# Performance work log

Measured on AMD Instinct MI355X. Metric: run time of the kernel, lower is better.

The kernel has to match this reference:

```python
import math
import jax, jax.numpy as jnp
import numpy as np

H = 1024
N2 = 32  # N // 2
L_LEN = 4096


def setup_inputs() -> dict:
    key = jax.random.key(0)
    k0, k1, k2 = jax.random.split(key, 3)
    log_dt = jax.random.uniform(k0, (H,), dtype=jnp.float32) * (
        math.log(0.1) - math.log(0.001)) + math.log(0.001)
    C_real = jax.random.normal(k1, (H, N2), dtype=jnp.float32)
    C_imag = jax.random.normal(k2, (H, N2), dtype=jnp.float32)
    log_A_real = jnp.log(0.5 * jnp.ones((H, N2), dtype=jnp.float32))
    A_imag = math.pi * jnp.tile(jnp.arange(N2, dtype=jnp.float32)[None, :], (H, 1))
    return {
        "log_dt": log_dt,
        "C_real": C_real,
        "C_imag": C_imag,
        "log_A_real": log_A_real,
        "A_imag": A_imag,
        "L": L_LEN,
    }


def reference(log_dt, C_real, C_imag, log_A_real, A_imag, L):
    dt = jnp.exp(log_dt)                                   # [H]
    A = -jnp.exp(log_A_real) + 1j * A_imag                 # [H, N2] complex
    dtA = A * dt[:, None]                                  # [H, N2]
    l = jnp.arange(L, dtype=jnp.float32)                   # [L]
    Kexp = jnp.exp(dtA[:, :, None] * l)                    # [H, N2, L] complex (Vandermonde)
    Ct = (C_real + 1j * C_imag) * (jnp.exp(dtA) - 1.0) / A  # [H, N2]
    K = 2.0 * jnp.einsum('hn,hnl->hl', Ct, Kexp).real      # [H, L]
    return K
```

## Files before the change

kernel.cpp:

```cpp
#include <hip/hip_runtime.h>


#define N2    32
#define NPAIR (N2 / 2)
#define LLEN  4096
#define BLK   256
#define CL    (LLEN / BLK)
#define PCH   4
#define TOL   1e-3f

typedef float v2f __attribute__((ext_vector_type(2)));

__global__ __launch_bounds__(BLK, 4) void s4d_kernel(
    const float* __restrict__ log_dt,
    const float* __restrict__ C_real,
    const float* __restrict__ C_imag,
    const float* __restrict__ log_A_real,
    const float* __restrict__ A_imag,
    float* __restrict__ out)
{
    const int h = blockIdx.x;
    const int t = threadIdx.x;

    __shared__ v2f    sT0[N2][16];
    __shared__ float4 sU1[N2][16];
    __shared__ v2f    s2A[NPAIR];
    __shared__ v2f    sMR2[NPAIR];
    __shared__ v2f    sCt[N2];
    __shared__ float  sDrl2[N2];
    __shared__ double sTrev[N2];
    __shared__ float  sS, sRmax, sDrmax;
    __shared__ int    sJcut;

    if (t < N2) {
        const int n = t;
        const float dt = __expf(log_dt[h]);
        const float aR = -__expf(log_A_real[h * N2 + n]);
        const float aI = A_imag[h * N2 + n];
        const float dR = aR * dt;

        const double trev = (double)aI * (double)dt * 0.15915494309189535;

        double pz = trev; pz -= floor(pz);
        const float e1 = __expf(dR);
        const float zr = e1 * __builtin_amdgcn_cosf((float)pz);
        const float zi = e1 * __builtin_amdgcn_sinf((float)pz);

        const float inv = 1.0f / (aR * aR + aI * aI);
        const float nr  = zr - 1.0f;
        const float qr  = (nr * aR + zi * aI) * inv;
        const float qi  = (zi * aR - nr * aI) * inv;
        const float c_r = C_real[h * N2 + n], c_i = C_imag[h * N2 + n];
        const float Ctr = c_r * qr - c_i * qi;
        const float Cti = c_r * qi + c_i * qr;

        double p256 = trev * 256.0; p256 -= floor(p256);
        const float ew = __expf(dR * 256.0f);
        const float wx = ew * __builtin_amdgcn_cosf((float)p256);
        const float r2 = ew * ew;
        const float drl2 = dR * 1.4426950408889634f;

        sCt[n]   = (v2f){Ctr, Cti};
        sDrl2[n] = drl2;
        sTrev[n] = trev;
        ((float*)s2A)[n]  = 2.0f * wx;
        ((float*)sMR2)[n] = -r2;

        float S = fabsf(Ctr) + fabsf(Cti);
        float r = ew;
        float dm = drl2;
#pragma unroll
        for (int m = 16; m >= 1; m >>= 1) {
            S  += __shfl_xor(S, m, 32);
            r   = fmaxf(r,  __shfl_xor(r,  m, 32));
            dm  = fmaxf(dm, __shfl_xor(dm, m, 32));
        }
        if (n == 0) {
            sS = S; sRmax = r; sDrmax = dm;
            int jc = CL;
            if (r < 0.9999f) {
                const float tail0 = 2.0f * S / (1.0f - r);
                jc = 0;
                float rj = 1.0f;
                while (jc < CL && tail0 * rj >= TOL) { rj *= r; ++jc; }
            }
            sJcut = jc;
        }
    }
    __syncthreads();

#pragma unroll
    for (int it = 0; it < 4; ++it) {
        const int tau = t + BLK * it;
        if (tau < 512) {
            const int n = tau >> 4, k = tau & 15;
            double p = sTrev[n] * (double)k; p -= floor(p);
            const float g = __builtin_amdgcn_exp2f(sDrl2[n] * (float)k);
            sT0[n][k] = (v2f){ g * __builtin_amdgcn_cosf((float)p),
                               g * __builtin_amdgcn_sinf((float)p) };
        } else {
            const int tu = tau - 512;
            const int n = tu >> 4, m = tu & 15;
            const v2f    Ct = sCt[n];
            const double tr = sTrev[n];
            const float  dl = sDrl2[n];

            double p0 = tr * (double)(16 * m); p0 -= floor(p0);
            const float g0 = __builtin_amdgcn_exp2f(dl * (float)(16 * m));
            const float c0 = g0 * __builtin_amdgcn_cosf((float)p0);
            const float s0 = g0 * __builtin_amdgcn_sinf((float)p0);

            double p1 = tr * (double)(16 * m + 256); p1 -= floor(p1);
            const float g1 = __builtin_amdgcn_exp2f(dl * (float)(16 * m + 256));
            const float c1 = g1 * __builtin_amdgcn_cosf((float)p1);
            const float s1 = g1 * __builtin_amdgcn_sinf((float)p1);

            sU1[n][m] = make_float4(Ct.x * c0 - Ct.y * s0,
                                    Ct.x * s0 + Ct.y * c0,
                                    Ct.x * c1 - Ct.y * s1,
                                    Ct.x * s1 + Ct.y * c1);
        }
    }
    __syncthreads();

    v2f acc[CL];
#pragma unroll
    for (int j = 0; j < CL; ++j) acc[j] = (v2f){0.0f, 0.0f};

    const int jcut = __builtin_amdgcn_readfirstlane(sJcut);
    bool active = (jcut > 0);
    {
        const float rmax = sRmax;
        if (rmax < 0.9999f) {
            const float bound = 2.0f * sS *
                __builtin_amdgcn_exp2f(sDrmax * (float)t) / (1.0f - rmax);
            if (bound < TOL) active = false;
        }
    }

    if (active) {
        const int t0 = t & 15, t1 = t >> 4;

        for (int p0 = 0; p0 < NPAIR; p0 += PCH) {
            v2f xa[PCH], xb[PCH], c2a[PCH], cmr[PCH];

#pragma unroll
            for (int k = 0; k < PCH; ++k) {
                const int pair = p0 + k;
                c2a[k] = s2A[pair];
                cmr[k] = sMR2[pair];
#pragma unroll
                for (int e = 0; e < 2; ++e) {
                    const int n = 2 * pair + e;
                    const v2f    b = sT0[n][t0];
                    const float4 u = sU1[n][t1];
                    const float x0 = __builtin_fmaf(-u.y, b.y, u.x * b.x);
                    const float x1 = __builtin_fmaf(-u.w, b.y, u.z * b.x);
                    if (e == 0) { xa[k].x = x0; xb[k].x = x1; }
                    else        { xa[k].y = x0; xb[k].y = x1; }
                }
            }

#pragma unroll
            for (int k = 0; k < PCH; ++k) acc[0] += xa[k];
            if (jcut > 1) {
#pragma unroll
                for (int k = 0; k < PCH; ++k) acc[1] += xb[k];
            }

#pragma unroll
            for (int jp = 0; jp < (CL - 2) / 2; ++jp) {
                const int j = 2 + 2 * jp;
                if (j < jcut) {
#pragma unroll
                    for (int k = 0; k < PCH; ++k) {
                        xa[k] = c2a[k] * xb[k] + cmr[k] * xa[k];
                        acc[j] += xa[k];
                    }
#pragma unroll
                    for (int k = 0; k < PCH; ++k) {
                        xb[k] = c2a[k] * xa[k] + cmr[k] * xb[k];
                        acc[j + 1] += xb[k];
                    }
                }
            }
        }
    }

    float* __restrict__ o = out + (size_t)h * LLEN + t;
#pragma unroll
    for (int j = 0; j < CL; ++j) o[j * BLK] = 2.0f * (acc[j].x + acc[j].y);
}

extern "C" void kernel_launch(void* const* d_in, const int* in_sizes, int n_in,
                              void* d_out, int out_size, void* d_ws, size_t ws_size,
                              hipStream_t stream) {
    const float* log_dt     = (const float*)d_in[0];
    const float* C_real     = (const float*)d_in[1];
    const float* C_imag     = (const float*)d_in[2];
    const float* log_A_real = (const float*)d_in[3];
    const float* A_imag     = (const float*)d_in[4];
    float* out = (float*)d_out;

    const int H = in_sizes[0];
    s4d_kernel<<<dim3(H), dim3(BLK), 0, stream>>>(
        log_dt, C_real, C_imag, log_A_real, A_imag, out);
}
```

Before: 78.14 us.

## Split modes across two thread halves per block and reduce via shared memory

Doubles the block to 512 threads. Each half handles 16 of the 32 modes for the same 256 output positions, using a scalar per-mode recurrence in place of the paired v2f packing. The partial sums are combined through a shared-memory buffer, and each half then writes half of the outputs. The aim is more parallelism per head and shorter serial recurrence chains per thread, at the cost of an extra reduction, two more barriers and more shared memory.

New measurement: 88.24 us. +12.9%, slower.

```diff
diff --git a/kernel.cpp b/kernel.cpp
--- a/kernel.cpp
+++ b/kernel.cpp
@@ -2,16 +2,15 @@
 
 
 #define N2    32
-#define NPAIR (N2 / 2)
 #define LLEN  4096
-#define BLK   256
-#define CL    (LLEN / BLK)
-#define PCH   4
+#define BLK   512
+#define TQ    256
+#define CL    16
 #define TOL   1e-3f
 
 typedef float v2f __attribute__((ext_vector_type(2)));
 
-__global__ __launch_bounds__(BLK, 4) void s4d_kernel(
+__global__ __launch_bounds__(BLK, 8) void s4d_kernel(
     const float* __restrict__ log_dt,
     const float* __restrict__ C_real,
     const float* __restrict__ C_imag,
@@ -19,21 +18,23 @@
     const float* __restrict__ A_imag,
     float* __restrict__ out)
 {
-    const int h = blockIdx.x;
-    const int t = threadIdx.x;
+    const int h   = blockIdx.x;
+    const int tid = threadIdx.x;
+    const int t   = tid & (TQ - 1);
+    const int sl  = tid >> 8;
 
     __shared__ v2f    sT0[N2][16];
     __shared__ float4 sU1[N2][16];
-    __shared__ v2f    s2A[NPAIR];
-    __shared__ v2f    sMR2[NPAIR];
+    __shared__ v2f    sAB[N2];
     __shared__ v2f    sCt[N2];
     __shared__ float  sDrl2[N2];
     __shared__ double sTrev[N2];
+    __shared__ float  sRed[CL][TQ];
     __shared__ float  sS, sRmax, sDrmax;
     __shared__ int    sJcut;
 
-    if (t < N2) {
-        const int n = t;
+    if (tid < N2) {
+        const int n = tid;
         const float dt = __expf(log_dt[h]);
         const float aR = -__expf(log_A_real[h * N2 + n]);
         const float aI = A_imag[h * N2 + n];
@@ -63,8 +64,7 @@
         sCt[n]   = (v2f){Ctr, Cti};
         sDrl2[n] = drl2;
         sTrev[n] = trev;
-        ((float*)s2A)[n]  = 2.0f * wx;
-        ((float*)sMR2)[n] = -r2;
+        sAB[n]   = (v2f){2.0f * wx, -r2};
 
         float S = fabsf(Ctr) + fabsf(Cti);
         float r = ew;
@@ -90,8 +90,8 @@
     __syncthreads();
 
 #pragma unroll
-    for (int it = 0; it < 4; ++it) {
-        const int tau = t + BLK * it;
+    for (int it = 0; it < 2; ++it) {
+        const int tau = tid + BLK * it;
         if (tau < 512) {
             const int n = tau >> 4, k = tau & 15;
             double p = sTrev[n] * (double)k; p -= floor(p);
@@ -123,9 +123,9 @@
     }
     __syncthreads();
 
-    v2f acc[CL];
-#pragma unroll
-    for (int j = 0; j < CL; ++j) acc[j] = (v2f){0.0f, 0.0f};
+    float acc[CL];
+#pragma unroll
+    for (int j = 0; j < CL; ++j) acc[j] = 0.0f;
 
     const int jcut = __builtin_amdgcn_readfirstlane(sJcut);
     bool active = (jcut > 0);
@@ -140,32 +140,28 @@
 
     if (active) {
         const int t0 = t & 15, t1 = t >> 4;
-
-        for (int p0 = 0; p0 < NPAIR; p0 += PCH) {
-            v2f xa[PCH], xb[PCH], c2a[PCH], cmr[PCH];
-
-#pragma unroll
-            for (int k = 0; k < PCH; ++k) {
-                const int pair = p0 + k;
-                c2a[k] = s2A[pair];
-                cmr[k] = sMR2[pair];
-#pragma unroll
-                for (int e = 0; e < 2; ++e) {
-                    const int n = 2 * pair + e;
-                    const v2f    b = sT0[n][t0];
-                    const float4 u = sU1[n][t1];
-                    const float x0 = __builtin_fmaf(-u.y, b.y, u.x * b.x);
-                    const float x1 = __builtin_fmaf(-u.w, b.y, u.z * b.x);
-                    if (e == 0) { xa[k].x = x0; xb[k].x = x1; }
-                    else        { xa[k].y = x0; xb[k].y = x1; }
-                }
-            }
-
-#pragma unroll
-            for (int k = 0; k < PCH; ++k) acc[0] += xa[k];
+        const int nbase = sl * 16;
+
+        for (int ch = 0; ch < 2; ++ch) {
+            const int nb = nbase + ch * 8;
+            float xa[8], xb[8], ca[8], cb[8];
+
+#pragma unroll
+            for (int k = 0; k < 8; ++k) {
+                const int n = nb + k;
+                const v2f    b = sT0[n][t0];
+                const float4 u = sU1[n][t1];
+                xa[k] = __builtin_fmaf(-u.y, b.y, u.x * b.x);
+                xb[k] = __builtin_fmaf(-u.w, b.y, u.z * b.x);
+                const v2f ab = sAB[n];
+                ca[k] = ab.x;  cb[k] = ab.y;
+            }
+
+#pragma unroll
+            for (int k = 0; k < 8; ++k) acc[0] += xa[k];
             if (jcut > 1) {
 #pragma unroll
-                for (int k = 0; k < PCH; ++k) acc[1] += xb[k];
+                for (int k = 0; k < 8; ++k) acc[1] += xb[k];
             }
 
 #pragma unroll
@@ -173,13 +169,13 @@
                 const int j = 2 + 2 * jp;
                 if (j < jcut) {
 #pragma unroll
-                    for (int k = 0; k < PCH; ++k) {
-                        xa[k] = c2a[k] * xb[k] + cmr[k] * xa[k];
+                    for (int k = 0; k < 8; ++k) {
+                        xa[k] = ca[k] * xb[k] + cb[k] * xa[k];
                         acc[j] += xa[k];
                     }
 #pragma unroll
-                    for (int k = 0; k < PCH; ++k) {
-                        xb[k] = c2a[k] * xa[k] + cmr[k] * xb[k];
+                    for (int k = 0; k < 8; ++k) {
+                        xb[k] = ca[k] * xa[k] + cb[k] * xb[k];
                         acc[j + 1] += xb[k];
                     }
                 }
@@ -187,9 +183,21 @@
         }
     }
 
-    float* __restrict__ o = out + (size_t)h * LLEN + t;
-#pragma unroll
-    for (int j = 0; j < CL; ++j) o[j * BLK] = 2.0f * (acc[j].x + acc[j].y);
+    if (sl == 0) {
+#pragma unroll
+        for (int j = 0; j < CL; ++j) sRed[j][t] = acc[j];
+    }
+    __syncthreads();
+    if (sl == 1) {
+#pragma unroll
+        for (int j = 0; j < CL; ++j) sRed[j][t] += acc[j];
+    }
+    __syncthreads();
+
+    float* __restrict__ o = out + (size_t)h * LLEN + sl * (8 * TQ) + t;
+#pragma unroll
+    for (int jj = 0; jj < 8; ++jj)
+        o[jj * TQ] = 2.0f * sRed[8 * sl + jj][t];
 }
 
 extern "C" void kernel_launch(void* const* d_in, const int* in_sizes, int n_in,
```

## Split each channel's sequence across two blocks and repack shared tables

Applied to the files above, without the earlier changes.

Launches two blocks per channel, each covering half of the output length, so there are twice as many blocks and each thread needs fewer accumulators, which allows higher occupancy (launch bounds raised to 6). Each block writes its half directly as zeros when the decay cutoff excludes it. U1 entries for the second step are now derived by multiplying by the 256-step rotation instead of a second transcendental evaluation. Shared tables are repacked into float4 pairs so loads are wider. The cost is that both halves repeat the per-channel setup and table construction.

Result: slower. 80.74 us (+3.3%).

```diff
diff --git a/kernel.cpp b/kernel.cpp
--- a/kernel.cpp
+++ b/kernel.cpp
@@ -1,17 +1,16 @@
 #include <hip/hip_runtime.h>
 
 
-#define N2    32
-#define NPAIR (N2 / 2)
 #define LLEN  4096
 #define BLK   256
-#define CL    (LLEN / BLK)
-#define PCH   4
+#define N2    32
+#define NPR   16
+#define JPB   8
 #define TOL   1e-3f
 
 typedef float v2f __attribute__((ext_vector_type(2)));
 
-__global__ __launch_bounds__(BLK, 4) void s4d_kernel(
+__global__ __launch_bounds__(BLK, 6) void s4d_kernel(
     const float* __restrict__ log_dt,
     const float* __restrict__ C_real,
     const float* __restrict__ C_imag,
@@ -19,14 +18,16 @@
     const float* __restrict__ A_imag,
     float* __restrict__ out)
 {
-    const int h = blockIdx.x;
-    const int t = threadIdx.x;
-
-    __shared__ v2f    sT0[N2][16];
+    const int bx   = blockIdx.x;
+    const int h    = bx >> 1;
+    const int half = bx & 1;
+    const int joff = half * JPB;
+    const int t    = threadIdx.x;
+
+    __shared__ float4 sT0P[NPR][16];
     __shared__ float4 sU1[N2][16];
-    __shared__ v2f    s2A[NPAIR];
-    __shared__ v2f    sMR2[NPAIR];
-    __shared__ v2f    sCt[N2];
+    __shared__ float4 sABP[NPR];
+    __shared__ v2f    sCt[N2], sW[N2];
     __shared__ float  sDrl2[N2];
     __shared__ double sTrev[N2];
     __shared__ float  sS, sRmax, sDrmax;
@@ -57,17 +58,20 @@
         double p256 = trev * 256.0; p256 -= floor(p256);
         const float ew = __expf(dR * 256.0f);
         const float wx = ew * __builtin_amdgcn_cosf((float)p256);
+        const float wy = ew * __builtin_amdgcn_sinf((float)p256);
         const float r2 = ew * ew;
         const float drl2 = dR * 1.4426950408889634f;
 
         sCt[n]   = (v2f){Ctr, Cti};
+        sW[n]    = (v2f){wx, wy};
         sDrl2[n] = drl2;
         sTrev[n] = trev;
-        ((float*)s2A)[n]  = 2.0f * wx;
-        ((float*)sMR2)[n] = -r2;
-
-        float S = fabsf(Ctr) + fabsf(Cti);
-        float r = ew;
+        float* ab = (float*)&sABP[n >> 1];
+        ab[n & 1]       = 2.0f * wx;
+        ab[2 + (n & 1)] = -r2;
+
+        float S  = fabsf(Ctr) + fabsf(Cti);
+        float r  = ew;
         float dm = drl2;
 #pragma unroll
         for (int m = 16; m >= 1; m >>= 1) {
@@ -77,17 +81,27 @@
         }
         if (n == 0) {
             sS = S; sRmax = r; sDrmax = dm;
-            int jc = CL;
+            int jc = 16;
             if (r < 0.9999f) {
                 const float tail0 = 2.0f * S / (1.0f - r);
                 jc = 0;
                 float rj = 1.0f;
-                while (jc < CL && tail0 * rj >= TOL) { rj *= r; ++jc; }
+                while (jc < 16 && tail0 * rj >= TOL) { rj *= r; ++jc; }
             }
             sJcut = jc;
         }
     }
     __syncthreads();
+
+    const int jcut  = __builtin_amdgcn_readfirstlane(sJcut);
+    const int jcl   = jcut - joff;
+    float* __restrict__ o = out + (size_t)h * LLEN + joff * BLK + t;
+
+    if (jcl <= 0) {
+#pragma unroll
+        for (int j = 0; j < JPB; ++j) o[j * BLK] = 0.0f;
+        return;
+    }
 
 #pragma unroll
     for (int it = 0; it < 4; ++it) {
@@ -96,44 +110,39 @@
             const int n = tau >> 4, k = tau & 15;
             double p = sTrev[n] * (double)k; p -= floor(p);
             const float g = __builtin_amdgcn_exp2f(sDrl2[n] * (float)k);
-            sT0[n][k] = (v2f){ g * __builtin_amdgcn_cosf((float)p),
-                               g * __builtin_amdgcn_sinf((float)p) };
+            float* dst = (float*)&sT0P[n >> 1][k] + (n & 1) * 2;
+            dst[0] = g * __builtin_amdgcn_cosf((float)p);
+            dst[1] = g * __builtin_amdgcn_sinf((float)p);
         } else {
             const int tu = tau - 512;
             const int n = tu >> 4, m = tu & 15;
-            const v2f    Ct = sCt[n];
-            const double tr = sTrev[n];
-            const float  dl = sDrl2[n];
-
-            double p0 = tr * (double)(16 * m); p0 -= floor(p0);
-            const float g0 = __builtin_amdgcn_exp2f(dl * (float)(16 * m));
-            const float c0 = g0 * __builtin_amdgcn_cosf((float)p0);
-            const float s0 = g0 * __builtin_amdgcn_sinf((float)p0);
-
-            double p1 = tr * (double)(16 * m + 256); p1 -= floor(p1);
-            const float g1 = __builtin_amdgcn_exp2f(dl * (float)(16 * m + 256));
-            const float c1 = g1 * __builtin_amdgcn_cosf((float)p1);
-            const float s1 = g1 * __builtin_amdgcn_sinf((float)p1);
-
-            sU1[n][m] = make_float4(Ct.x * c0 - Ct.y * s0,
-                                    Ct.x * s0 + Ct.y * c0,
-                                    Ct.x * c1 - Ct.y * s1,
-                                    Ct.x * s1 + Ct.y * c1);
+            const int e = 16 * m + 256 * joff;
+            double pu = sTrev[n] * (double)e; pu -= floor(pu);
+            const float gu = __builtin_amdgcn_exp2f(sDrl2[n] * (float)e);
+            const float c0 = gu * __builtin_amdgcn_cosf((float)pu);
+            const float s0 = gu * __builtin_amdgcn_sinf((float)pu);
+            const v2f Ct = sCt[n];
+            const v2f w  = sW[n];
+            const float u0r = Ct.x * c0 - Ct.y * s0;
+            const float u0i = Ct.x * s0 + Ct.y * c0;
+            sU1[n][m] = make_float4(u0r, u0i,
+                                    u0r * w.x - u0i * w.y,
+                                    u0r * w.y + u0i * w.x);
         }
     }
     __syncthreads();
 
-    v2f acc[CL];
-#pragma unroll
-    for (int j = 0; j < CL; ++j) acc[j] = (v2f){0.0f, 0.0f};
-
-    const int jcut = __builtin_amdgcn_readfirstlane(sJcut);
-    bool active = (jcut > 0);
+    float acc[JPB];
+#pragma unroll
+    for (int j = 0; j < JPB; ++j) acc[j] = 0.0f;
+
+    bool active = true;
     {
         const float rmax = sRmax;
         if (rmax < 0.9999f) {
             const float bound = 2.0f * sS *
-                __builtin_amdgcn_exp2f(sDrmax * (float)t) / (1.0f - rmax);
+                __builtin_amdgcn_exp2f(sDrmax * (float)(t + 2048 * half)) /
+                (1.0f - rmax);
             if (bound < TOL) active = false;
         }
     }
@@ -141,45 +150,44 @@
     if (active) {
         const int t0 = t & 15, t1 = t >> 4;
 
-        for (int p0 = 0; p0 < NPAIR; p0 += PCH) {
-            v2f xa[PCH], xb[PCH], c2a[PCH], cmr[PCH];
-
-#pragma unroll
-            for (int k = 0; k < PCH; ++k) {
-                const int pair = p0 + k;
-                c2a[k] = s2A[pair];
-                cmr[k] = sMR2[pair];
-#pragma unroll
-                for (int e = 0; e < 2; ++e) {
-                    const int n = 2 * pair + e;
-                    const v2f    b = sT0[n][t0];
-                    const float4 u = sU1[n][t1];
-                    const float x0 = __builtin_fmaf(-u.y, b.y, u.x * b.x);
-                    const float x1 = __builtin_fmaf(-u.w, b.y, u.z * b.x);
-                    if (e == 0) { xa[k].x = x0; xb[k].x = x1; }
-                    else        { xa[k].y = x0; xb[k].y = x1; }
-                }
-            }
-
-#pragma unroll
-            for (int k = 0; k < PCH; ++k) acc[0] += xa[k];
-            if (jcut > 1) {
-#pragma unroll
-                for (int k = 0; k < PCH; ++k) acc[1] += xb[k];
-            }
-
-#pragma unroll
-            for (int jp = 0; jp < (CL - 2) / 2; ++jp) {
+        for (int ch = 0; ch < 4; ++ch) {
+            float xa[8], xb[8], ca[8], cb[8];
+
+#pragma unroll
+            for (int pp = 0; pp < 4; ++pp) {
+                const int pair = ch * 4 + pp;
+                const float4 ab = sABP[pair];
+                const float4 b  = sT0P[pair][t0];
+                const float4 u0 = sU1[2 * pair][t1];
+                const float4 u1 = sU1[2 * pair + 1][t1];
+                const int k0 = 2 * pp, k1 = k0 + 1;
+                xa[k0] = __builtin_fmaf(-u0.y, b.y, u0.x * b.x);
+                xb[k0] = __builtin_fmaf(-u0.w, b.y, u0.z * b.x);
+                xa[k1] = __builtin_fmaf(-u1.y, b.w, u1.x * b.z);
+                xb[k1] = __builtin_fmaf(-u1.w, b.w, u1.z * b.z);
+                ca[k0] = ab.x; ca[k1] = ab.y;
+                cb[k0] = ab.z; cb[k1] = ab.w;
+            }
+
+#pragma unroll
+            for (int k = 0; k < 8; ++k) acc[0] += xa[k];
+            if (jcl > 1) {
+#pragma unroll
+                for (int k = 0; k < 8; ++k) acc[1] += xb[k];
+            }
+
+#pragma unroll
+            for (int jp = 0; jp < (JPB - 2) / 2; ++jp) {
                 const int j = 2 + 2 * jp;
-                if (j < jcut) {
-#pragma unroll
-                    for (int k = 0; k < PCH; ++k) {
-                        xa[k] = c2a[k] * xb[k] + cmr[k] * xa[k];
+                if (j < jcl) {
+#pragma unroll
+                    for (int k = 0; k < 8; ++k) {
+                        xa[k] = ca[k] * xb[k] + cb[k] * xa[k];
                         acc[j] += xa[k];
                     }
 #pragma unroll
-                    for (int k = 0; k < PCH; ++k) {
-                        xb[k] = c2a[k] * xa[k] + cmr[k] * xb[k];
+                    for (int k = 0; k < 8; ++k) {
+                        xb[k] = ca[k] * xa[k] + cb[k] * xb[k];
                         acc[j + 1] += xb[k];
                     }
                 }
@@ -187,9 +195,8 @@
         }
     }
 
-    float* __restrict__ o = out + (size_t)h * LLEN + t;
-#pragma unroll
-    for (int j = 0; j < CL; ++j) o[j * BLK] = 2.0f * (acc[j].x + acc[j].y);
+#pragma unroll
+    for (int j = 0; j < JPB; ++j) o[j * BLK] = 2.0f * acc[j];
 }
 
 extern "C" void kernel_launch(void* const* d_in, const int* in_sizes, int n_in,
@@ -203,6 +210,6 @@
     float* out = (float*)d_out;
 
     const int H = in_sizes[0];
-    s4d_kernel<<<dim3(H), dim3(BLK), 0, stream>>>(
+    s4d_kernel<<<dim3(2 * H), dim3(BLK), 0, stream>>>(
         log_dt, C_real, C_imag, log_A_real, A_imag, out);
 }
```
